# Kernel optimization log

Measured on AMD Instinct MI355X. Metric: run time of the kernel, lower is better.

## Reference

```python
import jax, jax.numpy as jnp
import numpy as np

D_MODEL, D_FF, NUM_EXPERTS, RANK, TOP_K = 1024, 4096, 8, 16, 2
B, S = 8, 2048


def _expert_ffn(h, wi_w, wo_w, A, Bm):
    # h: [B,S,D]; wi_w: [F,D]; wo_w: [D,F]; A: [R,D]; Bm: [F,R]
    inter = jnp.einsum('bsd,fd->bsf', h, wi_w)
    lora = jnp.einsum('bsr,fr->bsf', jnp.einsum('bsd,rd->bsr', h, A), Bm)
    inter = jax.nn.relu(inter + lora)
    return jnp.einsum('bsf,df->bsd', inter, wo_w)


def setup_inputs() -> dict:
    key = jax.random.key(0)
    ks = jax.random.split(key, 8)
    hidden_states = jax.random.normal(ks[0], (B, S, D_MODEL), dtype=jnp.float32)
    wi_w = jax.random.normal(ks[1], (D_FF, D_MODEL), dtype=jnp.float32) * (1.0 / np.sqrt(D_MODEL))
    wo_w = jax.random.normal(ks[2], (D_MODEL, D_FF), dtype=jnp.float32) * (1.0 / np.sqrt(D_FF))
    # kaiming-uniform-ish A; B random (zeros in init, randomized for a meaningful kernel baseline)
    lora_As = jax.random.uniform(ks[3], (NUM_EXPERTS, RANK, D_MODEL), dtype=jnp.float32, minval=-1.0, maxval=1.0) / np.sqrt(D_MODEL)
    lora_Bs = jax.random.normal(ks[4], (NUM_EXPERTS, D_FF, RANK), dtype=jnp.float32) * 0.02
    top_k_indices = jnp.arange(TOP_K, dtype=jnp.int32)  # task-level selected experts, shape [top_k]
    top_k_values = jax.random.uniform(ks[5], (TOP_K,), dtype=jnp.float32)
    return {'hidden_states': hidden_states, 'wi_w': wi_w, 'wo_w': wo_w,
            'lora_As': lora_As, 'lora_Bs': lora_Bs,
            'top_k_indices': top_k_indices, 'top_k_values': top_k_values}


def reference(hidden_states, wi_w, wo_w, lora_As, lora_Bs, top_k_indices, top_k_values):
    # Task-level top-k: each selected expert runs a full LoRA-augmented FFN over
    # all tokens, scaled by its scalar mixed routing weight, then summed.
    # sum_k v_k * ffn_{idx_k}(h) == sum_i (sum_{k: idx_k=i} v_k) * ffn_i(h)  (matches torch loop)
    out = jnp.zeros_like(hidden_states)
    for k in range(top_k_values.shape[0]):
        A = jnp.take(lora_As, top_k_indices[k], axis=0)
        Bm = jnp.take(lora_Bs, top_k_indices[k], axis=0)
        out = out + top_k_values[k] * _expert_ffn(hidden_states, wi_w, wo_w, A, Bm)
    return out
```

## Files before the change

kernel.cpp:

```cpp
#include <hip/hip_runtime.h>
#include <hip/hip_bf16.h>
#include <cstdint>
#include <cstddef>

#define D_MODEL 1024
#define D_FF    4096
#define RANK    16
#define NTOK    16384

typedef __attribute__((ext_vector_type(8))) __bf16 bf16x8;
typedef __attribute__((ext_vector_type(4))) float  f32x4;

using gas_t = const __attribute__((address_space(1))) void*;
using las_t = __attribute__((address_space(3))) void*;

__device__ __forceinline__ unsigned short f2bf(float f) {
    unsigned int u = __builtin_bit_cast(unsigned int, f);
    u += 0x7fffu + ((u >> 16) & 1u);
    return (unsigned short)(u >> 16);
}

__device__ __forceinline__ void gload_lds16(const unsigned short* g, unsigned short* l) {
    __builtin_amdgcn_global_load_lds((gas_t)g, (las_t)l, 16, 0, 0);
}

__global__ void cast_kernel(const float* __restrict__ in, unsigned short* __restrict__ out, int n4) {
    int i = blockIdx.x * blockDim.x + threadIdx.x;
    int stride = gridDim.x * blockDim.x;
    for (; i < n4; i += stride) {
        float4 v = reinterpret_cast<const float4*>(in)[i];
        ushort4 o;
        o.x = f2bf(v.x); o.y = f2bf(v.y); o.z = f2bf(v.z); o.w = f2bf(v.w);
        reinterpret_cast<ushort4*>(out)[i] = o;
    }
}

__global__ void prep_kernel(const float* __restrict__ Bs, const float* __restrict__ As,
                            const int* __restrict__ idx,
                            unsigned short* __restrict__ bcat, unsigned short* __restrict__ acatg) {
    int i = blockIdx.x * blockDim.x + threadIdx.x;
    if (i < D_FF * 32) {
        int f = i >> 5, kk = i & 31, e = kk >> 4, r = kk & 15;
        bcat[i] = f2bf(Bs[(size_t)idx[e] * D_FF * RANK + (size_t)f * RANK + r]);
    } else {
        int j = i - D_FF * 32;
        int row = j >> 10, col = j & 1023, e = row >> 4, r = row & 15;
        acatg[j] = f2bf(As[(size_t)idx[e] * RANK * D_MODEL + r * D_MODEL + col]);
    }
}

__global__ void lora_t_v2(const float* __restrict__ h,
                          const unsigned short* __restrict__ acatg,
                          unsigned short* __restrict__ tcat,
                          unsigned short* __restrict__ hbf) {
    const int tid = threadIdx.x, lane = tid & 63, w = tid >> 6;
    const int tok0 = blockIdx.x * 64 + w * 16;
    const int lr = lane & 15, kc = lane >> 4;
    f32x4 acc0 = {}, acc1 = {};
    const size_t rowoff = (size_t)(tok0 + lr) * D_MODEL;
    #pragma unroll 4
    for (int kt = 0; kt < 32; ++kt) {
        const int k0 = kt * 32 + kc * 8;
        float4 u0 = *reinterpret_cast<const float4*>(h + rowoff + k0);
        float4 u1 = *reinterpret_cast<const float4*>(h + rowoff + k0 + 4);
        union { bf16x8 v; unsigned short s[8]; } af;
        af.s[0] = f2bf(u0.x); af.s[1] = f2bf(u0.y); af.s[2] = f2bf(u0.z); af.s[3] = f2bf(u0.w);
        af.s[4] = f2bf(u1.x); af.s[5] = f2bf(u1.y); af.s[6] = f2bf(u1.z); af.s[7] = f2bf(u1.w);
        *reinterpret_cast<bf16x8*>(&hbf[rowoff + k0]) = af.v;
        bf16x8 b0 = *reinterpret_cast<const bf16x8*>(&acatg[(size_t)lr * D_MODEL + k0]);
        bf16x8 b1 = *reinterpret_cast<const bf16x8*>(&acatg[(size_t)(16 + lr) * D_MODEL + k0]);
        acc0 = __builtin_amdgcn_mfma_f32_16x16x32_bf16(af.v, b0, acc0, 0, 0, 0);
        acc1 = __builtin_amdgcn_mfma_f32_16x16x32_bf16(af.v, b1, acc1, 0, 0, 0);
    }
    #pragma unroll
    for (int j = 0; j < 4; ++j) {
        tcat[(size_t)(tok0 + kc * 4 + j) * 32 + lr]      = f2bf(acc0[j]);
        tcat[(size_t)(tok0 + kc * 4 + j) * 32 + 16 + lr] = f2bf(acc1[j]);
    }
}

template<int KDIM, int EPI, int OSTRIDE, int GN>
__launch_bounds__(512, 2)
__global__ void gemm256(const unsigned short* __restrict__ A,
                        const unsigned short* __restrict__ Bm,
                        float* __restrict__ outF,
                        unsigned short* __restrict__ outBf,
                        const unsigned short* __restrict__ tcat,
                        const unsigned short* __restrict__ bcat,
                        const float* __restrict__ topv) {
    __shared__ unsigned short lds[2][2][2][128 * 64];
    const int tid  = threadIdx.x;
    const int lane = tid & 63;
    const int wid  = tid >> 6;
    const int wr   = wid >> 2;
    const int wc   = wid & 3;
    const int lr   = lane & 15;
    const int hi   = lane >> 4;
    const int swz  = (lane & 7) << 3;

    const int nwg  = gridDim.x;
    const int orig = blockIdx.x;
    const int wg   = (orig & 7) * (nwg >> 3) + (orig >> 3);
    const int bm0  = (wg / GN) * 256;
    const int bn0  = (wg % GN) * 256;

    constexpr int NKT = KDIM / 64;
    constexpr int NT2 = NKT / 2;

    f32x4 acc[8][4] = {};
    bf16x8 aF[8], b0[4], b1[4];

    auto stage = [&](int buf, int mat, int half, const unsigned short* src, int kt) {
        const int row0 = (mat == 0 ? bm0 : bn0) + half * 128;
        const int k0 = kt * 64;
        #pragma unroll
        for (int p = 0; p < 2; ++p) {
            const int L = p * 8192 + tid * 16;
            const int r = L >> 7;
            const int c = (L & 127) >> 1;
            const int gc = k0 + (c ^ ((r & 7) << 3));
            gload_lds16(src + (size_t)(row0 + r) * KDIM + gc,
                        &lds[buf][mat][half][0] + (L >> 1));
        }
    };
    auto readA = [&](int buf, int qm) {
        #pragma unroll
        for (int fr = 0; fr < 4; ++fr)
            #pragma unroll
            for (int ks = 0; ks < 2; ++ks)
                aF[fr * 2 + ks] = *reinterpret_cast<const bf16x8*>(
                    &lds[buf][0][wr][(qm * 64 + fr * 16 + lr) * 64 + ((ks * 32 + hi * 8) ^ swz)]);
    };
    auto readB = [&](int buf, int qn, bf16x8* bb) {
        #pragma unroll
        for (int fc = 0; fc < 2; ++fc)
            #pragma unroll
            for (int ks = 0; ks < 2; ++ks)
                bb[fc * 2 + ks] = *reinterpret_cast<const bf16x8*>(
                    &lds[buf][1][wc >> 1][((wc & 1) * 64 + qn * 32 + fc * 16 + lr) * 64
                                          + ((ks * 32 + hi * 8) ^ swz)]);
    };
    auto mfma16 = [&](int qm, int qn, const bf16x8* bb) {
        #pragma unroll
        for (int fr = 0; fr < 4; ++fr)
            #pragma unroll
            for (int fc = 0; fc < 2; ++fc)
                #pragma unroll
                for (int ks = 0; ks < 2; ++ks)
                    acc[qm * 4 + fr][qn * 2 + fc] = __builtin_amdgcn_mfma_f32_16x16x32_bf16(
                        aF[fr * 2 + ks], bb[fc * 2 + ks], acc[qm * 4 + fr][qn * 2 + fc], 0, 0, 0);
    };

#define BAR() __builtin_amdgcn_s_barrier()
#define WAIT_LGKM() do { asm volatile("s_waitcnt lgkmcnt(0)" ::: "memory"); \
                         __builtin_amdgcn_sched_barrier(0); } while (0)
#define WAIT_VM(n) do { asm volatile("s_waitcnt vmcnt(" #n ")" ::: "memory"); \
                        __builtin_amdgcn_sched_barrier(0); } while (0)
#define PRIO_MFMA(qm, qn, bb) do { __builtin_amdgcn_s_setprio(1); mfma16(qm, qn, bb); \
                                   __builtin_amdgcn_s_setprio(0); } while (0)

    stage(0, 0, 0, A, 0);  stage(0, 0, 1, A, 0);
    stage(0, 1, 0, Bm, 0); stage(0, 1, 1, Bm, 0);
    stage(1, 1, 0, Bm, 1); stage(1, 1, 1, Bm, 1);
    WAIT_VM(4);
    BAR();

    #pragma unroll 1
    for (int it = 0; it < NT2; ++it) {
        const int t1 = 2 * it + 1;
        const int t2 = (2 * it + 2 < NKT) ? 2 * it + 2 : NKT - 1;
        const int t3 = (2 * it + 3 < NKT) ? 2 * it + 3 : NKT - 1;
        readA(0, 0); readB(0, 0, b0);
        stage(1, 0, 0, A, t1);
        BAR(); WAIT_LGKM(); PRIO_MFMA(0, 0, b0); BAR();
        readB(0, 1, b1);
        stage(1, 0, 1, A, t1);
        BAR(); WAIT_LGKM(); PRIO_MFMA(0, 1, b1); BAR();
        readA(0, 1);
        stage(0, 1, 0, Bm, t2);
        BAR(); WAIT_LGKM(); PRIO_MFMA(1, 0, b0); BAR();
        stage(0, 1, 1, Bm, t2);
        BAR(); PRIO_MFMA(1, 1, b1); WAIT_VM(4); BAR();
        readA(1, 0); readB(1, 0, b0);
        stage(0, 0, 0, A, t2);
        BAR(); WAIT_LGKM(); PRIO_MFMA(0, 0, b0); BAR();
        readB(1, 1, b1);
        stage(0, 0, 1, A, t2);
        BAR(); WAIT_LGKM(); PRIO_MFMA(0, 1, b1); BAR();
        readA(1, 1);
        stage(1, 1, 0, Bm, t3);
        BAR(); WAIT_LGKM(); PRIO_MFMA(1, 0, b0); BAR();
        stage(1, 1, 1, Bm, t3);
        BAR(); PRIO_MFMA(1, 1, b1); WAIT_VM(4); BAR();
    }
    asm volatile("s_waitcnt vmcnt(0)" ::: "memory");
    __builtin_amdgcn_sched_barrier(0);
    BAR();

    const int rbase = bm0 + wr * 128 + hi * 4;
    const int cbase = bn0 + wc * 64 + lr;

    if constexpr (EPI == 1) {
        const float v0 = topv[0], v1 = topv[1];
        const bf16x8 z8 = {};
        bf16x8 bl0[4], bl1[4];
        #pragma unroll
        for (int ni = 0; ni < 4; ++ni) {
            const int f = cbase + ni * 16;
            bf16x8 bfull = *reinterpret_cast<const bf16x8*>(&bcat[(size_t)f * 32 + hi * 8]);
            bl0[ni] = (hi < 2) ? bfull : z8;
            bl1[ni] = (hi < 2) ? z8 : bfull;
        }
        #pragma unroll
        for (int mi = 0; mi < 8; ++mi) {
            const int mrow = bm0 + wr * 128 + mi * 16 + lr;
            const bf16x8 alo = *reinterpret_cast<const bf16x8*>(&tcat[(size_t)mrow * 32 + hi * 8]);
            #pragma unroll
            for (int ni = 0; ni < 4; ++ni) {
                const f32x4 zz = {};
                f32x4 l0 = __builtin_amdgcn_mfma_f32_16x16x32_bf16(alo, bl0[ni], zz, 0, 0, 0);
                f32x4 l1 = __builtin_amdgcn_mfma_f32_16x16x32_bf16(alo, bl1[ni], zz, 0, 0, 0);
                #pragma unroll
                for (int j = 0; j < 4; ++j) {
                    float z = acc[mi][ni][j];
                    float c = v0 * fmaxf(z + l0[j], 0.f) + v1 * fmaxf(z + l1[j], 0.f);
                    outBf[(size_t)(rbase + mi * 16 + j) * OSTRIDE + cbase + ni * 16] = f2bf(c);
                }
            }
        }
    } else {
        #pragma unroll
        for (int mi = 0; mi < 8; ++mi)
            #pragma unroll
            for (int ni = 0; ni < 4; ++ni)
                #pragma unroll
                for (int j = 0; j < 4; ++j)
                    outF[(size_t)(rbase + mi * 16 + j) * OSTRIDE + cbase + ni * 16] = acc[mi][ni][j];
    }
#undef BAR
#undef WAIT_LGKM
#undef WAIT_VM
#undef PRIO_MFMA
}

extern "C" void kernel_launch(void* const* d_in, const int* in_sizes, int n_in,
                              void* d_out, int out_size, void* d_ws, size_t ws_size,
                              hipStream_t stream) {
    const float* h    = (const float*)d_in[0];
    const float* wi   = (const float*)d_in[1];
    const float* wo   = (const float*)d_in[2];
    const float* As   = (const float*)d_in[3];
    const float* Bs   = (const float*)d_in[4];
    const int*   idx  = (const int*)d_in[5];
    const float* topv = (const float*)d_in[6];
    float* out = (float*)d_out;

    char* ws = (char*)d_ws;
    unsigned short* hbf   = (unsigned short*)(ws);
    unsigned short* wibf  = (unsigned short*)(ws + 33554432);
    unsigned short* wobf  = (unsigned short*)(ws + 41943040);
    unsigned short* tcat  = (unsigned short*)(ws + 50331648);
    unsigned short* bcat  = (unsigned short*)(ws + 51380224);
    unsigned short* acatg = (unsigned short*)(ws + 51642368);
    unsigned short* comb  = (unsigned short*)(ws + 51707904);

    prep_kernel<<<640, 256, 0, stream>>>(Bs, As, idx, bcat, acatg);
    lora_t_v2<<<NTOK / 64, 256, 0, stream>>>(h, acatg, tcat, hbf);
    cast_kernel<<<1024, 256, 0, stream>>>(wi, wibf, (D_FF * D_MODEL) / 4);
    cast_kernel<<<1024, 256, 0, stream>>>(wo, wobf, (D_MODEL * D_FF) / 4);

    gemm256<D_MODEL, 1, D_FF, 16><<<dim3(64 * 16), 512, 0, stream>>>(
        hbf, wibf, nullptr, comb, tcat, bcat, topv);
    gemm256<D_FF, 0, D_MODEL, 4><<<dim3(64 * 4), 512, 0, stream>>>(
        comb, wobf, out, nullptr, nullptr, nullptr, nullptr);
}
```

Baseline: 289.6 us.

## Prefetch next LDS fragments into double-buffered registers during MFMA phases

Adds a second A-fragment register set so each phase's LDS reads for the next MFMA block are issued before the current MFMA block runs, instead of reading and then waiting. The loop is rotated so the first fragments are loaded before it and the next iteration's fragments at the end of each half. This aims to hide LDS read latency behind matrix instructions. It costs more VGPRs, which may reduce occupancy or cause spills, and the final iteration issues an extra redundant read.

```diff
diff --git a/kernel.cpp b/kernel.cpp
--- a/kernel.cpp
+++ b/kernel.cpp
@@ -108,7 +108,7 @@
     constexpr int NT2 = NKT / 2;
 
     f32x4 acc[8][4] = {};
-    bf16x8 aF[8], b0[4], b1[4];
+    bf16x8 aF[8], aF2[8], b0[4], b1[4];
 
     auto stage = [&](int buf, int mat, int half, const unsigned short* src, int kt) {
         const int row0 = (mat == 0 ? bm0 : bn0) + half * 128;
@@ -123,12 +123,12 @@
                         &lds[buf][mat][half][0] + (L >> 1));
         }
     };
-    auto readA = [&](int buf, int qm) {
+    auto readA = [&](int buf, int qm, bf16x8* dst) {
         #pragma unroll
         for (int fr = 0; fr < 4; ++fr)
             #pragma unroll
             for (int ks = 0; ks < 2; ++ks)
-                aF[fr * 2 + ks] = *reinterpret_cast<const bf16x8*>(
+                dst[fr * 2 + ks] = *reinterpret_cast<const bf16x8*>(
                     &lds[buf][0][wr][(qm * 64 + fr * 16 + lr) * 64 + ((ks * 32 + hi * 8) ^ swz)]);
     };
     auto readB = [&](int buf, int qn, bf16x8* bb) {
@@ -140,7 +140,7 @@
                     &lds[buf][1][wc >> 1][((wc & 1) * 64 + qn * 32 + fc * 16 + lr) * 64
                                           + ((ks * 32 + hi * 8) ^ swz)]);
     };
-    auto mfma16 = [&](int qm, int qn, const bf16x8* bb) {
+    auto mfma16 = [&](const bf16x8* aa, int qm, int qn, const bf16x8* bb) {
         #pragma unroll
         for (int fr = 0; fr < 4; ++fr)
             #pragma unroll
@@ -148,53 +148,72 @@
                 #pragma unroll
                 for (int ks = 0; ks < 2; ++ks)
                     acc[qm * 4 + fr][qn * 2 + fc] = __builtin_amdgcn_mfma_f32_16x16x32_bf16(
-                        aF[fr * 2 + ks], bb[fc * 2 + ks], acc[qm * 4 + fr][qn * 2 + fc], 0, 0, 0);
+                        aa[fr * 2 + ks], bb[fc * 2 + ks], acc[qm * 4 + fr][qn * 2 + fc], 0, 0, 0);
     };
 
 #define BAR() __builtin_amdgcn_s_barrier()
-#define WAIT_LGKM() do { asm volatile("s_waitcnt lgkmcnt(0)" ::: "memory"); \
-                         __builtin_amdgcn_sched_barrier(0); } while (0)
-#define WAIT_VM(n) do { asm volatile("s_waitcnt vmcnt(" #n ")" ::: "memory"); \
-                        __builtin_amdgcn_sched_barrier(0); } while (0)
-#define PRIO_MFMA(qm, qn, bb) do { __builtin_amdgcn_s_setprio(1); mfma16(qm, qn, bb); \
-                                   __builtin_amdgcn_s_setprio(0); } while (0)
+#define SCHED0() __builtin_amdgcn_sched_barrier(0)
+#define WAIT_LGKM() do { asm volatile("s_waitcnt lgkmcnt(0)" ::: "memory"); SCHED0(); } while (0)
+#define WAIT_VM(n) do { asm volatile("s_waitcnt vmcnt(" #n ")" ::: "memory"); SCHED0(); } while (0)
+#define PRIO_MFMA(aa, qm, qn, bb) do { __builtin_amdgcn_s_setprio(1); mfma16(aa, qm, qn, bb); \
+                                       __builtin_amdgcn_s_setprio(0); } while (0)
 
     stage(0, 0, 0, A, 0);  stage(0, 0, 1, A, 0);
     stage(0, 1, 0, Bm, 0); stage(0, 1, 1, Bm, 0);
     stage(1, 1, 0, Bm, 1); stage(1, 1, 1, Bm, 1);
     WAIT_VM(4);
     BAR();
+    readA(0, 0, aF);
+    readB(0, 0, b0);
 
     #pragma unroll 1
     for (int it = 0; it < NT2; ++it) {
         const int t1 = 2 * it + 1;
         const int t2 = (2 * it + 2 < NKT) ? 2 * it + 2 : NKT - 1;
         const int t3 = (2 * it + 3 < NKT) ? 2 * it + 3 : NKT - 1;
-        readA(0, 0); readB(0, 0, b0);
         stage(1, 0, 0, A, t1);
-        BAR(); WAIT_LGKM(); PRIO_MFMA(0, 0, b0); BAR();
-        readB(0, 1, b1);
+        BAR(); WAIT_LGKM();
+        readB(0, 1, b1); SCHED0();
+        PRIO_MFMA(aF, 0, 0, b0);
+        BAR();
         stage(1, 0, 1, A, t1);
-        BAR(); WAIT_LGKM(); PRIO_MFMA(0, 1, b1); BAR();
-        readA(0, 1);
+        BAR(); WAIT_LGKM();
+        readA(0, 1, aF2); SCHED0();
+        PRIO_MFMA(aF, 0, 1, b1);
+        BAR();
         stage(0, 1, 0, Bm, t2);
-        BAR(); WAIT_LGKM(); PRIO_MFMA(1, 0, b0); BAR();
+        BAR(); WAIT_LGKM();
+        PRIO_MFMA(aF2, 1, 0, b0);
+        BAR();
         stage(0, 1, 1, Bm, t2);
-        BAR(); PRIO_MFMA(1, 1, b1); WAIT_VM(4); BAR();
-        readA(1, 0); readB(1, 0, b0);
+        WAIT_VM(4);
+        BAR();
+        readA(1, 0, aF); readB(1, 0, b0); SCHED0();
+        PRIO_MFMA(aF2, 1, 1, b1);
+        BAR();
         stage(0, 0, 0, A, t2);
-        BAR(); WAIT_LGKM(); PRIO_MFMA(0, 0, b0); BAR();
-        readB(1, 1, b1);
+        BAR(); WAIT_LGKM();
+        readB(1, 1, b1); SCHED0();
+        PRIO_MFMA(aF, 0, 0, b0);
+        BAR();
         stage(0, 0, 1, A, t2);
-        BAR(); WAIT_LGKM(); PRIO_MFMA(0, 1, b1); BAR();
-        readA(1, 1);
+        BAR(); WAIT_LGKM();
+        readA(1, 1, aF2); SCHED0();
+        PRIO_MFMA(aF, 0, 1, b1);
+        BAR();
         stage(1, 1, 0, Bm, t3);
-        BAR(); WAIT_LGKM(); PRIO_MFMA(1, 0, b0); BAR();
+        BAR(); WAIT_LGKM();
+        PRIO_MFMA(aF2, 1, 0, b0);
+        BAR();
         stage(1, 1, 1, Bm, t3);
-        BAR(); PRIO_MFMA(1, 1, b1); WAIT_VM(4); BAR();
+        WAIT_VM(4);
+        BAR();
+        readA(0, 0, aF); readB(0, 0, b0); SCHED0();
+        PRIO_MFMA(aF2, 1, 1, b1);
+        BAR();
     }
     asm volatile("s_waitcnt vmcnt(0)" ::: "memory");
-    __builtin_amdgcn_sched_barrier(0);
+    SCHED0();
     BAR();
 
     const int rbase = bm0 + wr * 128 + hi * 4;
@@ -238,6 +257,7 @@
                     outF[(size_t)(rbase + mi * 16 + j) * OSTRIDE + cbase + ni * 16] = acc[mi][ni][j];
     }
 #undef BAR
+#undef SCHED0
 #undef WAIT_LGKM
 #undef WAIT_VM
 #undef PRIO_MFMA
```

After: 440.5 us. +52.1%, slower.

## Make first GEMM persistent over four M tiles with cross-tile prefetch

Applied to the files above, without the earlier changes.

The first GEMM now launches 256 workgroups instead of 1024, and each one loops over four consecutive 256-row M tiles for a fixed N tile. The last k-iteration of each tile prefetches the first k-slices of the next tile, so the pipeline does not drain and refill between tiles. The B-side LoRA fragments are loaded once per workgroup. This cuts launch and prologue overhead and can improve reuse of the B tile in L2. The trade-off is coarser load balance with only 256 workgroups, and the epilogue stores of each tile are now serialized with the next tile's main loop.

```diff
diff --git a/kernel.cpp b/kernel.cpp
--- a/kernel.cpp
+++ b/kernel.cpp
@@ -79,7 +79,7 @@
     }
 }
 
-template<int KDIM, int EPI, int OSTRIDE, int GN>
+template<int KDIM, int EPI, int OSTRIDE, int GN, int NTM>
 __launch_bounds__(512, 2)
 __global__ void gemm256(const unsigned short* __restrict__ A,
                         const unsigned short* __restrict__ Bm,
@@ -101,8 +101,8 @@
     const int nwg  = gridDim.x;
     const int orig = blockIdx.x;
     const int wg   = (orig & 7) * (nwg >> 3) + (orig >> 3);
-    const int bm0  = (wg / GN) * 256;
     const int bn0  = (wg % GN) * 256;
+    int       bm0  = (wg / GN) * (NTM * 256);
 
     constexpr int NKT = KDIM / 64;
     constexpr int NT2 = NKT / 2;
@@ -110,9 +110,7 @@
     f32x4 acc[8][4] = {};
     bf16x8 aF[8], b0[4], b1[4];
 
-    auto stage = [&](int buf, int mat, int half, const unsigned short* src, int kt) {
-        const int row0 = (mat == 0 ? bm0 : bn0) + half * 128;
-        const int k0 = kt * 64;
+    auto stage = [&](int buf, int mat, int half, const unsigned short* src, int row0, int k0) {
         #pragma unroll
         for (int p = 0; p < 2; ++p) {
             const int L = p * 8192 + tid * 16;
@@ -159,51 +157,18 @@
 #define PRIO_MFMA(qm, qn, bb) do { __builtin_amdgcn_s_setprio(1); mfma16(qm, qn, bb); \
                                    __builtin_amdgcn_s_setprio(0); } while (0)
 
-    stage(0, 0, 0, A, 0);  stage(0, 0, 1, A, 0);
-    stage(0, 1, 0, Bm, 0); stage(0, 1, 1, Bm, 0);
-    stage(1, 1, 0, Bm, 1); stage(1, 1, 1, Bm, 1);
+    stage(0, 0, 0, A, bm0, 0);        stage(0, 0, 1, A, bm0 + 128, 0);
+    stage(0, 1, 0, Bm, bn0, 0);       stage(0, 1, 1, Bm, bn0 + 128, 0);
+    stage(1, 1, 0, Bm, bn0, 64);      stage(1, 1, 1, Bm, bn0 + 128, 64);
     WAIT_VM(4);
     BAR();
 
-    #pragma unroll 1
-    for (int it = 0; it < NT2; ++it) {
-        const int t1 = 2 * it + 1;
-        const int t2 = (2 * it + 2 < NKT) ? 2 * it + 2 : NKT - 1;
-        const int t3 = (2 * it + 3 < NKT) ? 2 * it + 3 : NKT - 1;
-        readA(0, 0); readB(0, 0, b0);
-        stage(1, 0, 0, A, t1);
-        BAR(); WAIT_LGKM(); PRIO_MFMA(0, 0, b0); BAR();
-        readB(0, 1, b1);
-        stage(1, 0, 1, A, t1);
-        BAR(); WAIT_LGKM(); PRIO_MFMA(0, 1, b1); BAR();
-        readA(0, 1);
-        stage(0, 1, 0, Bm, t2);
-        BAR(); WAIT_LGKM(); PRIO_MFMA(1, 0, b0); BAR();
-        stage(0, 1, 1, Bm, t2);
-        BAR(); PRIO_MFMA(1, 1, b1); WAIT_VM(4); BAR();
-        readA(1, 0); readB(1, 0, b0);
-        stage(0, 0, 0, A, t2);
-        BAR(); WAIT_LGKM(); PRIO_MFMA(0, 0, b0); BAR();
-        readB(1, 1, b1);
-        stage(0, 0, 1, A, t2);
-        BAR(); WAIT_LGKM(); PRIO_MFMA(0, 1, b1); BAR();
-        readA(1, 1);
-        stage(1, 1, 0, Bm, t3);
-        BAR(); WAIT_LGKM(); PRIO_MFMA(1, 0, b0); BAR();
-        stage(1, 1, 1, Bm, t3);
-        BAR(); PRIO_MFMA(1, 1, b1); WAIT_VM(4); BAR();
-    }
-    asm volatile("s_waitcnt vmcnt(0)" ::: "memory");
-    __builtin_amdgcn_sched_barrier(0);
-    BAR();
-
-    const int rbase = bm0 + wr * 128 + hi * 4;
+    float v0 = 0.f, v1 = 0.f;
     const int cbase = bn0 + wc * 64 + lr;
-
+    bf16x8 bl0[4], bl1[4];
     if constexpr (EPI == 1) {
-        const float v0 = topv[0], v1 = topv[1];
+        v0 = topv[0]; v1 = topv[1];
         const bf16x8 z8 = {};
-        bf16x8 bl0[4], bl1[4];
         #pragma unroll
         for (int ni = 0; ni < 4; ++ni) {
             const int f = cbase + ni * 16;
@@ -211,32 +176,81 @@
             bl0[ni] = (hi < 2) ? bfull : z8;
             bl1[ni] = (hi < 2) ? z8 : bfull;
         }
-        #pragma unroll
-        for (int mi = 0; mi < 8; ++mi) {
-            const int mrow = bm0 + wr * 128 + mi * 16 + lr;
-            const bf16x8 alo = *reinterpret_cast<const bf16x8*>(&tcat[(size_t)mrow * 32 + hi * 8]);
+    }
+
+    #pragma unroll 1
+    for (int tl = 0; tl < NTM; ++tl) {
+        const int bm_next = (tl + 1 < NTM) ? bm0 + 256 : bm0;
+
+        #pragma unroll 1
+        for (int it = 0; it < NT2; ++it) {
+            const bool lastit = (it == NT2 - 1);
+            const int t1k = (2 * it + 1) * 64;
+            const int t2k = lastit ? 0  : (2 * it + 2) * 64;
+            const int t3k = lastit ? 64 : (2 * it + 3) * 64;
+            const int bmS = lastit ? bm_next : bm0;
+            readA(0, 0); readB(0, 0, b0);
+            stage(1, 0, 0, A, bm0, t1k);
+            BAR(); WAIT_LGKM(); PRIO_MFMA(0, 0, b0); BAR();
+            readB(0, 1, b1);
+            stage(1, 0, 1, A, bm0 + 128, t1k);
+            BAR(); WAIT_LGKM(); PRIO_MFMA(0, 1, b1); BAR();
+            readA(0, 1);
+            stage(0, 1, 0, Bm, bn0, t2k);
+            BAR(); WAIT_LGKM(); PRIO_MFMA(1, 0, b0); BAR();
+            stage(0, 1, 1, Bm, bn0 + 128, t2k);
+            BAR(); PRIO_MFMA(1, 1, b1); WAIT_VM(4); BAR();
+            readA(1, 0); readB(1, 0, b0);
+            stage(0, 0, 0, A, bmS, t2k);
+            BAR(); WAIT_LGKM(); PRIO_MFMA(0, 0, b0); BAR();
+            readB(1, 1, b1);
+            stage(0, 0, 1, A, bmS + 128, t2k);
+            BAR(); WAIT_LGKM(); PRIO_MFMA(0, 1, b1); BAR();
+            readA(1, 1);
+            stage(1, 1, 0, Bm, bn0, t3k);
+            BAR(); WAIT_LGKM(); PRIO_MFMA(1, 0, b0); BAR();
+            stage(1, 1, 1, Bm, bn0 + 128, t3k);
+            BAR(); PRIO_MFMA(1, 1, b1); WAIT_VM(4); BAR();
+        }
+
+        const int rbase = bm0 + wr * 128 + hi * 4;
+        if constexpr (EPI == 1) {
+            #pragma unroll
+            for (int mi = 0; mi < 8; ++mi) {
+                const int mrow = bm0 + wr * 128 + mi * 16 + lr;
+                const bf16x8 alo = *reinterpret_cast<const bf16x8*>(&tcat[(size_t)mrow * 32 + hi * 8]);
+                #pragma unroll
+                for (int ni = 0; ni < 4; ++ni) {
+                    const f32x4 zz = {};
+                    f32x4 l0 = __builtin_amdgcn_mfma_f32_16x16x32_bf16(alo, bl0[ni], zz, 0, 0, 0);
+                    f32x4 l1 = __builtin_amdgcn_mfma_f32_16x16x32_bf16(alo, bl1[ni], zz, 0, 0, 0);
+                    #pragma unroll
+                    for (int j = 0; j < 4; ++j) {
+                        float z = acc[mi][ni][j];
+                        float c = v0 * fmaxf(z + l0[j], 0.f) + v1 * fmaxf(z + l1[j], 0.f);
+                        outBf[(size_t)(rbase + mi * 16 + j) * OSTRIDE + cbase + ni * 16] = f2bf(c);
+                    }
+                }
+            }
+        } else {
+            #pragma unroll
+            for (int mi = 0; mi < 8; ++mi)
+                #pragma unroll
+                for (int ni = 0; ni < 4; ++ni)
+                    #pragma unroll
+                    for (int j = 0; j < 4; ++j)
+                        outF[(size_t)(rbase + mi * 16 + j) * OSTRIDE + cbase + ni * 16] = acc[mi][ni][j];
+        }
+        #pragma unroll
+        for (int mi = 0; mi < 8; ++mi)
             #pragma unroll
             for (int ni = 0; ni < 4; ++ni) {
                 const f32x4 zz = {};
-                f32x4 l0 = __builtin_amdgcn_mfma_f32_16x16x32_bf16(alo, bl0[ni], zz, 0, 0, 0);
-                f32x4 l1 = __builtin_amdgcn_mfma_f32_16x16x32_bf16(alo, bl1[ni], zz, 0, 0, 0);
-                #pragma unroll
-                for (int j = 0; j < 4; ++j) {
-                    float z = acc[mi][ni][j];
-                    float c = v0 * fmaxf(z + l0[j], 0.f) + v1 * fmaxf(z + l1[j], 0.f);
-                    outBf[(size_t)(rbase + mi * 16 + j) * OSTRIDE + cbase + ni * 16] = f2bf(c);
-                }
+                acc[mi][ni] = zz;
             }
-        }
-    } else {
-        #pragma unroll
-        for (int mi = 0; mi < 8; ++mi)
-            #pragma unroll
-            for (int ni = 0; ni < 4; ++ni)
-                #pragma unroll
-                for (int j = 0; j < 4; ++j)
-                    outF[(size_t)(rbase + mi * 16 + j) * OSTRIDE + cbase + ni * 16] = acc[mi][ni][j];
-    }
+        bm0 = bm_next;
+    }
+    asm volatile("s_waitcnt vmcnt(0)" ::: "memory");
 #undef BAR
 #undef WAIT_LGKM
 #undef WAIT_VM
@@ -269,8 +283,8 @@
     cast_kernel<<<1024, 256, 0, stream>>>(wi, wibf, (D_FF * D_MODEL) / 4);
     cast_kernel<<<1024, 256, 0, stream>>>(wo, wobf, (D_MODEL * D_FF) / 4);
 
-    gemm256<D_MODEL, 1, D_FF, 16><<<dim3(64 * 16), 512, 0, stream>>>(
+    gemm256<D_MODEL, 1, D_FF, 16, 4><<<dim3(256), 512, 0, stream>>>(
         hbf, wibf, nullptr, comb, tcat, bcat, topv);
-    gemm256<D_FF, 0, D_MODEL, 4><<<dim3(64 * 4), 512, 0, stream>>>(
+    gemm256<D_FF, 0, D_MODEL, 4, 1><<<dim3(256), 512, 0, stream>>>(
         comb, wobf, out, nullptr, nullptr, nullptr, nullptr);
 }
```

Measured after the change: 316.8 us. +9.4%, slower.
